# Kernel tuning notes

Measured on AMD Instinct MI355X. Metric: run time of the kernel, lower is better.

The kernel has to match this reference:

```python
import jax, jax.numpy as jnp
import numpy as np

B, J, D = 2048, 22, 128

def setup_inputs() -> dict:
    key = jax.random.key(0)
    k1, k2, k3 = jax.random.split(key, 3)
    src = jax.random.normal(k1, (B, J, D), dtype=jnp.float32)
    W = jax.random.normal(k2, (D, D), dtype=jnp.float32) * (1.0 / np.sqrt(D))
    b = jax.random.normal(k3, (D,), dtype=jnp.float32) * 0.01
    return {"src": src, "W": W, "b": b}

def reference(src, W, b):
    # Path-based accumulation sum_k (src[path[k+1]] - src[path[k]]) telescopes
    # to src[:, j, :] - src[:, i, :] for the shortest path i -> j.
    # pairwise[b, i, j, :] = src[b, j, :] - src[b, i, :]
    pairwise = src[:, None, :, :] - src[:, :, None, :]  # [B, J, J, D]
    # nn.Linear on last dim: x @ W^T + b
    return jnp.einsum('bijd,ed->bije', pairwise, W) + b
```

## Files before the change

kernel.cpp:

```cpp
#include <hip/hip_runtime.h>

#define NB 2048
#define NJ 22
#define ND 128
#define ROW4 (NJ * ND / 4)
#define YB4  (NJ * ND / 4)

typedef float f32x4 __attribute__((ext_vector_type(4)));

__global__ __launch_bounds__(256, 4) void gemm_y(
    const float* __restrict__ src, const float* __restrict__ W,
    float* __restrict__ Y) {
  __shared__ float srcS[NJ * ND];
  __shared__ float YS[NJ * ND];

  const int b = blockIdx.x;
  const int t = threadIdx.x;
  const float* srcB = src + (size_t)b * NJ * ND;

  for (int idx = t; idx < NJ * ND / 4; idx += 256) {
    reinterpret_cast<f32x4*>(srcS)[idx] =
        reinterpret_cast<const f32x4*>(srcB)[idx];
  }

  const int e  = t & 127;
  const int dh = t >> 7;

  float w[64];
  {
    const f32x4* Wrow = reinterpret_cast<const f32x4*>(W + e * ND + dh * 64);
#pragma unroll
    for (int k = 0; k < 16; ++k) {
      f32x4 v = Wrow[k];
      w[4 * k + 0] = v.x;
      w[4 * k + 1] = v.y;
      w[4 * k + 2] = v.z;
      w[4 * k + 3] = v.w;
    }
  }
  __syncthreads();

  for (int c = 0; c < 2; ++c) {
    float acc[11];
#pragma unroll
    for (int jj = 0; jj < 11; ++jj) {
      const int j = c * 11 + jj;
      const f32x4* s4 = reinterpret_cast<const f32x4*>(srcS + j * ND + dh * 64);
      float a = 0.f;
#pragma unroll
      for (int k = 0; k < 16; ++k) {
        f32x4 s = s4[k];
        a += s.x * w[4 * k + 0];
        a += s.y * w[4 * k + 1];
        a += s.z * w[4 * k + 2];
        a += s.w * w[4 * k + 3];
      }
      acc[jj] = a;
    }
    if (dh == 0) {
#pragma unroll
      for (int jj = 0; jj < 11; ++jj) YS[(c * 11 + jj) * ND + e] = acc[jj];
    }
    __syncthreads();
    if (dh == 1) {
#pragma unroll
      for (int jj = 0; jj < 11; ++jj) YS[(c * 11 + jj) * ND + e] += acc[jj];
    }
  }
  __syncthreads();

  f32x4* Yb4 = reinterpret_cast<f32x4*>(Y + (size_t)b * NJ * ND);
  const f32x4* YS4 = reinterpret_cast<const f32x4*>(YS);
  Yb4[t] = YS4[t];
  Yb4[t + 256] = YS4[t + 256];
  if (t < 192) Yb4[t + 512] = YS4[t + 512];
}

__global__ __launch_bounds__(256, 8) void expand(
    const float* __restrict__ Y, const float* __restrict__ bias,
    float* __restrict__ out) {
  __shared__ float YS[NJ * ND];

  const int b = blockIdx.x;
  const int t = threadIdx.x;

  const f32x4* Yb4 = reinterpret_cast<const f32x4*>(Y + (size_t)b * NJ * ND);
  f32x4* YS4w = reinterpret_cast<f32x4*>(YS);
  YS4w[t] = Yb4[t];
  YS4w[t + 256] = Yb4[t + 256];
  if (t < 192) YS4w[t + 512] = Yb4[t + 512];
  __syncthreads();

  const int e4 = t & 31;
  const int j0 = t >> 5;
  const f32x4* YS4 = reinterpret_cast<const f32x4*>(YS);
  const f32x4 bb4 = reinterpret_cast<const f32x4*>(bias)[e4];

  f32x4 yj0 = YS4[j0 * 32 + e4] + bb4;
  f32x4 yj1 = YS4[(j0 + 8) * 32 + e4] + bb4;
  f32x4 yj2 = {0.f, 0.f, 0.f, 0.f};
  if (j0 < 6) yj2 = YS4[(j0 + 16) * 32 + e4] + bb4;

  f32x4* outB4 = reinterpret_cast<f32x4*>(out + (size_t)b * NJ * NJ * ND);

  for (int ii = 0; ii < NJ; ++ii) {
    f32x4 yi = YS4[ii * 32 + e4];
    f32x4* outRow4 = outB4 + (size_t)ii * ROW4;
    outRow4[t] = yj0 - yi;
    outRow4[t + 256] = yj1 - yi;
    if (j0 < 6) outRow4[t + 512] = yj2 - yi;
  }
}

extern "C" void kernel_launch(void* const* d_in, const int* in_sizes, int n_in,
                              void* d_out, int out_size, void* d_ws, size_t ws_size,
                              hipStream_t stream) {
  const float* src  = (const float*)d_in[0];
  const float* W    = (const float*)d_in[1];
  const float* bias = (const float*)d_in[2];
  float* out = (float*)d_out;
  float* Yw  = (float*)d_ws;

  gemm_y<<<NB, 256, 0, stream>>>(src, W, Yw);
  expand<<<NB, 256, 0, stream>>>(Yw, bias, out);
}
```

Measured before the change: 135.8 us.

## Replace per-batch LDS expand kernel with flat grid-stride global expand

The expand kernel no longer stages each batch's Y into shared memory. It now runs a flat grid-stride loop over all output vec4 elements, reading Y[j] and Y[i] straight from global memory (mostly cache hits) and writing out in fully linear order. This drops the LDS staging and block barrier and makes the write stream contiguous across the whole grid, at the cost of integer divisions per element and twice as many global loads.

```diff
diff --git a/kernel.cpp b/kernel.cpp
--- a/kernel.cpp
+++ b/kernel.cpp
@@ -3,8 +3,10 @@
 #define NB 2048
 #define NJ 22
 #define ND 128
-#define ROW4 (NJ * ND / 4)
-#define YB4  (NJ * ND / 4)
+#define JD (NJ * ND)
+#define ROW4 (JD / 4)
+#define B4 (NJ * ROW4)
+#define TOT4 (NB * B4)
 
 typedef float f32x4 __attribute__((ext_vector_type(4)));
 
@@ -16,9 +18,9 @@
 
   const int b = blockIdx.x;
   const int t = threadIdx.x;
-  const float* srcB = src + (size_t)b * NJ * ND;
+  const float* srcB = src + (size_t)b * JD;
 
-  for (int idx = t; idx < NJ * ND / 4; idx += 256) {
+  for (int idx = t; idx < JD / 4; idx += 256) {
     reinterpret_cast<f32x4*>(srcS)[idx] =
         reinterpret_cast<const f32x4*>(srcB)[idx];
   }
@@ -32,10 +34,8 @@
 #pragma unroll
     for (int k = 0; k < 16; ++k) {
       f32x4 v = Wrow[k];
-      w[4 * k + 0] = v.x;
-      w[4 * k + 1] = v.y;
-      w[4 * k + 2] = v.z;
-      w[4 * k + 3] = v.w;
+      w[4 * k + 0] = v.x; w[4 * k + 1] = v.y;
+      w[4 * k + 2] = v.z; w[4 * k + 3] = v.w;
     }
   }
   __syncthreads();
@@ -69,46 +69,31 @@
   }
   __syncthreads();
 
-  f32x4* Yb4 = reinterpret_cast<f32x4*>(Y + (size_t)b * NJ * ND);
+  f32x4* Yb4 = reinterpret_cast<f32x4*>(Y + (size_t)b * JD);
   const f32x4* YS4 = reinterpret_cast<const f32x4*>(YS);
   Yb4[t] = YS4[t];
   Yb4[t + 256] = YS4[t + 256];
   if (t < 192) Yb4[t + 512] = YS4[t + 512];
 }
 
-__global__ __launch_bounds__(256, 8) void expand(
+__global__ __launch_bounds__(256) void expand_flat(
     const float* __restrict__ Y, const float* __restrict__ bias,
     float* __restrict__ out) {
-  __shared__ float YS[NJ * ND];
+  const int nthr = gridDim.x * blockDim.x;
+  const int q0 = blockIdx.x * blockDim.x + threadIdx.x;
+  const f32x4* Y4 = reinterpret_cast<const f32x4*>(Y);
+  f32x4* out4 = reinterpret_cast<f32x4*>(out);
+  const f32x4 bb = reinterpret_cast<const f32x4*>(bias)[q0 & 31];
 
-  const int b = blockIdx.x;
-  const int t = threadIdx.x;
-
-  const f32x4* Yb4 = reinterpret_cast<const f32x4*>(Y + (size_t)b * NJ * ND);
-  f32x4* YS4w = reinterpret_cast<f32x4*>(YS);
-  YS4w[t] = Yb4[t];
-  YS4w[t + 256] = Yb4[t + 256];
-  if (t < 192) YS4w[t + 512] = Yb4[t + 512];
-  __syncthreads();
-
-  const int e4 = t & 31;
-  const int j0 = t >> 5;
-  const f32x4* YS4 = reinterpret_cast<const f32x4*>(YS);
-  const f32x4 bb4 = reinterpret_cast<const f32x4*>(bias)[e4];
-
-  f32x4 yj0 = YS4[j0 * 32 + e4] + bb4;
-  f32x4 yj1 = YS4[(j0 + 8) * 32 + e4] + bb4;
-  f32x4 yj2 = {0.f, 0.f, 0.f, 0.f};
-  if (j0 < 6) yj2 = YS4[(j0 + 16) * 32 + e4] + bb4;
-
-  f32x4* outB4 = reinterpret_cast<f32x4*>(out + (size_t)b * NJ * NJ * ND);
-
-  for (int ii = 0; ii < NJ; ++ii) {
-    f32x4 yi = YS4[ii * 32 + e4];
-    f32x4* outRow4 = outB4 + (size_t)ii * ROW4;
-    outRow4[t] = yj0 - yi;
-    outRow4[t + 256] = yj1 - yi;
-    if (j0 < 6) outRow4[t + 512] = yj2 - yi;
+  for (int q = q0; q < TOT4; q += nthr) {
+    const int b = q / B4;
+    const int r = q - b * B4;
+    const int i = r / ROW4;
+    const int s = r - i * ROW4;
+    const int yb = b * ROW4;
+    f32x4 yj = Y4[yb + s];
+    f32x4 yi = Y4[yb + i * 32 + (q & 31)];
+    out4[q] = yj - yi + bb;
   }
 }
 
@@ -122,5 +107,5 @@
   float* Yw  = (float*)d_ws;
 
   gemm_y<<<NB, 256, 0, stream>>>(src, W, Yw);
-  expand<<<NB, 256, 0, stream>>>(Yw, bias, out);
+  expand_flat<<<2048, 256, 0, stream>>>(Yw, bias, out);
 }
```

Measured after the change: 160.2 us. +18.0%, slower.
